# Performance work log

Measured on AMD Instinct MI355X. Metric: run time of the kernel, lower is better.

## Reference

```python
import jax, jax.numpy as jnp
import numpy as np

N, D, E, EDGE_DIM = 50000, 128, 800000, 3
NEG_SLOPE = 0.2
LN_EPS = 1e-5


def setup_inputs() -> dict:
    key = jax.random.key(0)
    ks = jax.random.split(key, 12)
    s = 1.0 / np.sqrt(D)
    return {
        "x": jax.random.normal(ks[0], (N, D), jnp.float32),
        "edge_index": jax.random.randint(ks[1], (2, E), 0, N, jnp.int32),
        "edge_attr": jax.random.normal(ks[2], (E, EDGE_DIM), jnp.float32),
        "W_l": jax.random.normal(ks[3], (D, D), jnp.float32) * s,
        "b_l": jnp.zeros((D,), jnp.float32),
        "W_r": jax.random.normal(ks[4], (D, D), jnp.float32) * s,
        "b_r": jnp.zeros((D,), jnp.float32),
        "W_e": jax.random.normal(ks[5], (EDGE_DIM, D), jnp.float32) * (1.0 / np.sqrt(EDGE_DIM)),
        "att": jax.random.normal(ks[6], (D,), jnp.float32) * s,
        "bias": jnp.zeros((D,), jnp.float32),
        "res_weight": jnp.array(0.1, jnp.float32),
        "ln_gamma": jnp.ones((D,), jnp.float32),
        "ln_beta": jnp.zeros((D,), jnp.float32),
    }


def reference(x, edge_index, edge_attr, W_l, b_l, W_r, b_r, W_e, att, bias,
              res_weight, ln_gamma, ln_beta):
    src, dst = edge_index[0], edge_index[1]
    # GATv2: lin_l on source, lin_r on target (heads=1, concat=False)
    x_l = x @ W_l + b_l            # [N, D]
    x_r = x @ W_r + b_r            # [N, D]
    e_emb = edge_attr @ W_e        # [E, D]
    # per-edge attention logits
    m = x_l[src] + x_r[dst] + e_emb                      # [E, D]
    m = jnp.where(m > 0, m, NEG_SLOPE * m)               # leaky_relu(0.2)
    alpha = m @ att                                       # [E]
    # segment softmax over destination nodes
    seg_max = jax.ops.segment_max(alpha, dst, num_segments=N)
    seg_max = jnp.where(jnp.isfinite(seg_max), seg_max, 0.0)
    ex = jnp.exp(alpha - seg_max[dst])
    seg_sum = jax.ops.segment_sum(ex, dst, num_segments=N)
    alpha = ex / (seg_sum[dst] + 1e-16)                   # [E]
    # weighted aggregation of transformed source features (dropout off / eval)
    msgs = x_l[src] * alpha[:, None]                      # [E, D]
    out = jax.ops.segment_sum(msgs, dst, num_segments=N) + bias  # [N, D]
    # residual + LayerNorm
    out = x + res_weight * out
    mu = jnp.mean(out, axis=-1, keepdims=True)
    var = jnp.mean(jnp.square(out - mu), axis=-1, keepdims=True)
    out = (out - mu) * jax.lax.rsqrt(var + LN_EPS)
    return out * ln_gamma + ln_beta
```

## Files before the change

### kernel.cpp

```cpp
#include <hip/hip_runtime.h>
#include <hip/hip_bf16.h>

#define N_NODES 50000
#define DIM 128
#define N_EDGES 800000
#define NEG_SLOPE 0.2f
#define LN_EPS 1e-5f
#define SCAN_BS 256
#define NB_SCAN ((N_NODES + SCAN_BS - 1) / SCAN_BS)
#define PADCAP (N_EDGES + 4 * N_NODES)


__global__ __launch_bounds__(256) void lin_kernel(
    const float* __restrict__ x,
    const float* __restrict__ Wl, const float* __restrict__ bl,
    const float* __restrict__ Wr, const float* __restrict__ br,
    __hip_bfloat16* __restrict__ xl_bf, float* __restrict__ xr)
{
    __shared__ float xs[8][DIM];
    const int node0 = blockIdx.x * 8;
    const int t = threadIdx.x;
    for (int i = t; i < 8 * DIM; i += 256) {
        int n = node0 + (i >> 7);
        xs[i >> 7][i & 127] = (n < N_NODES) ? x[(size_t)n * DIM + (i & 127)] : 0.f;
    }
    __syncthreads();
    const int d = t & 127;
    const bool is_l = (t < 128);
    const float* W = is_l ? Wl : Wr;
    const float* b = is_l ? bl : br;
    float acc[8];
#pragma unroll
    for (int i = 0; i < 8; i++) acc[i] = b[d];
#pragma unroll 4
    for (int k = 0; k < DIM; k++) {
        float w = W[k * DIM + d];
#pragma unroll
        for (int i = 0; i < 8; i++) acc[i] += xs[i][k] * w;
    }
#pragma unroll
    for (int i = 0; i < 8; i++) {
        int n = node0 + i;
        if (n < N_NODES) {
            if (is_l) xl_bf[(size_t)n * DIM + d] = __float2bfloat16(acc[i]);
            else      xr[(size_t)n * DIM + d] = acc[i];
        }
    }
}

__global__ __launch_bounds__(256) void hist_kernel(const int* __restrict__ dst_idx,
                                                   int* __restrict__ cnt) {
    int i = blockIdx.x * 256 + threadIdx.x;
    int e = i * 4;
    if (e + 4 <= N_EDGES) {
        const int4 d4 = *(const int4*)(dst_idx + e);
        atomicAdd(&cnt[d4.x], 1);
        atomicAdd(&cnt[d4.y], 1);
        atomicAdd(&cnt[d4.z], 1);
        atomicAdd(&cnt[d4.w], 1);
    } else {
        for (; e < N_EDGES; ++e) atomicAdd(&cnt[dst_idx[e]], 1);
    }
}

__global__ __launch_bounds__(SCAN_BS) void scan1_kernel(int* __restrict__ cnt,
                                                        int* __restrict__ partials) {
    __shared__ int sh[SCAN_BS];
    const int i = blockIdx.x * SCAN_BS + threadIdx.x;
    const int deg = (i < N_NODES) ? cnt[i] : 0;
    const int v = (deg + 3) & ~3;
    sh[threadIdx.x] = v;
    __syncthreads();
    for (int off = 1; off < SCAN_BS; off <<= 1) {
        int u = (threadIdx.x >= off) ? sh[threadIdx.x - off] : 0;
        __syncthreads();
        sh[threadIdx.x] += u;
        __syncthreads();
    }
    if (i < N_NODES) cnt[i] = sh[threadIdx.x] - v;
    if (threadIdx.x == SCAN_BS - 1) partials[blockIdx.x] = sh[threadIdx.x];
}

__global__ __launch_bounds__(SCAN_BS) void scan2_kernel(int* __restrict__ partials) {
    __shared__ int sh[SCAN_BS];
    const int t = threadIdx.x;
    const int v = (t < NB_SCAN) ? partials[t] : 0;
    sh[t] = v;
    __syncthreads();
    for (int off = 1; off < SCAN_BS; off <<= 1) {
        int u = (t >= off) ? sh[t - off] : 0;
        __syncthreads();
        sh[t] += u;
        __syncthreads();
    }
    if (t < NB_SCAN) partials[t] = sh[t] - v;
}

__global__ __launch_bounds__(SCAN_BS) void scan3_kernel(int* __restrict__ cnt,
                                                        const int* __restrict__ partials,
                                                        int* __restrict__ cursor) {
    const int i = blockIdx.x * SCAN_BS + threadIdx.x;
    if (i < N_NODES) {
        int rs = cnt[i] + partials[blockIdx.x];
        cnt[i] = rs;
        cursor[i] = rs;
    }
}

__global__ __launch_bounds__(256) void scatter_kernel(
    const int* __restrict__ src_idx, const int* __restrict__ dst_idx,
    const float* __restrict__ ea,
    int* __restrict__ cursor, float4* __restrict__ packed) {
    int e = blockIdx.x * 256 + threadIdx.x;
    if (e >= N_EDGES) return;
    int pos = atomicAdd(&cursor[dst_idx[e]], 1);
    float4 p;
    p.x = ea[(size_t)e * 3 + 0];
    p.y = ea[(size_t)e * 3 + 1];
    p.z = ea[(size_t)e * 3 + 2];
    p.w = __int_as_float(src_idx[e]);
    packed[pos] = p;
}

__global__ __launch_bounds__(256) void fused_node_kernel(
    const float* __restrict__ x, const __hip_bfloat16* __restrict__ xl_bf,
    const int* __restrict__ row_start, const int* __restrict__ cursor,
    const float4* __restrict__ packed,
    const float* __restrict__ We, const float* __restrict__ att,
    const float* __restrict__ bias, const float* __restrict__ rw_p,
    const float* __restrict__ gamma, const float* __restrict__ beta,
    float* __restrict__ out)
{
    const int v = blockIdx.x * 4 + (threadIdx.x >> 6);
    const int lane = threadIdx.x & 63;
    if (v >= N_NODES) return;
    const int begin = row_start[v];
    const int end   = cursor[v];
    const size_t nb = (size_t)v * DIM + 2 * lane;
    const int loff = 2 * lane;
    const float2 xrv = *(const float2*)&out[nb];
    const float2 at  = *(const float2*)&att[loff];
    const float2 we0 = *(const float2*)&We[0 * DIM + loff];
    const float2 we1 = *(const float2*)&We[1 * DIM + loff];
    const float2 we2 = *(const float2*)&We[2 * DIM + loff];

    float m = -3.4e38f, s = 0.f, a0 = 0.f, a1 = 0.f;
    int pos = begin;
    const int full_end = begin + ((end - begin) & ~3);

    float4 pk0, pk1, pk2, pk3;
    unsigned xu0, xu1, xu2, xu3;
    if (pos < full_end) {
        pk0 = packed[pos];     pk1 = packed[pos + 1];
        pk2 = packed[pos + 2]; pk3 = packed[pos + 3];
        xu0 = *(const unsigned*)&xl_bf[(size_t)__float_as_int(pk0.w) * DIM + loff];
        xu1 = *(const unsigned*)&xl_bf[(size_t)__float_as_int(pk1.w) * DIM + loff];
        xu2 = *(const unsigned*)&xl_bf[(size_t)__float_as_int(pk2.w) * DIM + loff];
        xu3 = *(const unsigned*)&xl_bf[(size_t)__float_as_int(pk3.w) * DIM + loff];
    }

    while (pos < full_end) {
        const int npos = pos + 4;
        const bool more = npos < full_end;
        float4 nk0, nk1, nk2, nk3;
        if (more) {
            nk0 = packed[npos];     nk1 = packed[npos + 1];
            nk2 = packed[npos + 2]; nk3 = packed[npos + 3];
        }
        const float xl00 = __uint_as_float(xu0 << 16), xl10 = __uint_as_float(xu0 & 0xffff0000u);
        const float xl01 = __uint_as_float(xu1 << 16), xl11 = __uint_as_float(xu1 & 0xffff0000u);
        const float xl02 = __uint_as_float(xu2 << 16), xl12 = __uint_as_float(xu2 & 0xffff0000u);
        const float xl03 = __uint_as_float(xu3 << 16), xl13 = __uint_as_float(xu3 & 0xffff0000u);

        float P0, P1, P2, P3;
        {
            float t0, t1;
            t0 = xl00 + xrv.x + pk0.x * we0.x + pk0.y * we1.x + pk0.z * we2.x;
            t1 = xl10 + xrv.y + pk0.x * we0.y + pk0.y * we1.y + pk0.z * we2.y;
            t0 = t0 > 0.f ? t0 : NEG_SLOPE * t0;  t1 = t1 > 0.f ? t1 : NEG_SLOPE * t1;
            P0 = t0 * at.x + t1 * at.y;
            t0 = xl01 + xrv.x + pk1.x * we0.x + pk1.y * we1.x + pk1.z * we2.x;
            t1 = xl11 + xrv.y + pk1.x * we0.y + pk1.y * we1.y + pk1.z * we2.y;
            t0 = t0 > 0.f ? t0 : NEG_SLOPE * t0;  t1 = t1 > 0.f ? t1 : NEG_SLOPE * t1;
            P1 = t0 * at.x + t1 * at.y;
            t0 = xl02 + xrv.x + pk2.x * we0.x + pk2.y * we1.x + pk2.z * we2.x;
            t1 = xl12 + xrv.y + pk2.x * we0.y + pk2.y * we1.y + pk2.z * we2.y;
            t0 = t0 > 0.f ? t0 : NEG_SLOPE * t0;  t1 = t1 > 0.f ? t1 : NEG_SLOPE * t1;
            P2 = t0 * at.x + t1 * at.y;
            t0 = xl03 + xrv.x + pk3.x * we0.x + pk3.y * we1.x + pk3.z * we2.x;
            t1 = xl13 + xrv.y + pk3.x * we0.y + pk3.y * we1.y + pk3.z * we2.y;
            t0 = t0 > 0.f ? t0 : NEG_SLOPE * t0;  t1 = t1 > 0.f ? t1 : NEG_SLOPE * t1;
            P3 = t0 * at.x + t1 * at.y;
        }
        unsigned nu0, nu1, nu2, nu3;
        if (more) {
            nu0 = *(const unsigned*)&xl_bf[(size_t)__float_as_int(nk0.w) * DIM + loff];
            nu1 = *(const unsigned*)&xl_bf[(size_t)__float_as_int(nk1.w) * DIM + loff];
            nu2 = *(const unsigned*)&xl_bf[(size_t)__float_as_int(nk2.w) * DIM + loff];
            nu3 = *(const unsigned*)&xl_bf[(size_t)__float_as_int(nk3.w) * DIM + loff];
        }
        const float tA0 = __shfl_xor(P0, 1, 64);
        const float tA1 = __shfl_xor(P1, 1, 64);
        const float tB0 = __shfl_xor(P2, 1, 64);
        const float tB1 = __shfl_xor(P3, 1, 64);
        const bool b0 = (lane & 1);
        float A = b0 ? (P1 + tA1) : (P0 + tA0);
        float B = b0 ? (P3 + tB1) : (P2 + tB0);
        const float tA = __shfl_xor(A, 2, 64);
        const float tB = __shfl_xor(B, 2, 64);
        float C = (lane & 2) ? (B + tB) : (A + tA);
        C += __shfl_xor(C, 4, 64);
        C += __shfl_xor(C, 8, 64);
        C += __shfl_xor(C, 16, 64);
        C += __shfl_xor(C, 32, 64);
        const int base = lane & ~3;
        const float p0 = __shfl(C, base + 0, 64);
        const float p1 = __shfl(C, base + 1, 64);
        const float p2 = __shfl(C, base + 2, 64);
        const float p3 = __shfl(C, base + 3, 64);

        const float pm = fmaxf(fmaxf(p0, p1), fmaxf(p2, p3));
        if (pm <= m + 8.f) {
            const float w0 = __expf(p0 - m), w1 = __expf(p1 - m);
            const float w2 = __expf(p2 - m), w3 = __expf(p3 - m);
            s  += (w0 + w1) + (w2 + w3);
            a0 += w0 * xl00 + w1 * xl01 + w2 * xl02 + w3 * xl03;
            a1 += w0 * xl10 + w1 * xl11 + w2 * xl12 + w3 * xl13;
        } else {
            const float mn = fmaxf(m, pm);
            const float f  = __expf(m - mn);
            const float w0 = __expf(p0 - mn), w1 = __expf(p1 - mn);
            const float w2 = __expf(p2 - mn), w3 = __expf(p3 - mn);
            s  = s  * f + (w0 + w1) + (w2 + w3);
            a0 = a0 * f + w0 * xl00 + w1 * xl01 + w2 * xl02 + w3 * xl03;
            a1 = a1 * f + w0 * xl10 + w1 * xl11 + w2 * xl12 + w3 * xl13;
            m = mn;
        }
        pk0 = nk0; pk1 = nk1; pk2 = nk2; pk3 = nk3;
        xu0 = nu0; xu1 = nu1; xu2 = nu2; xu3 = nu3;
        pos = npos;
    }

    for (; pos < end; ++pos) {
        const float4 pk = packed[pos];
        const int sn = __float_as_int(pk.w);
        const unsigned xu = *(const unsigned*)&xl_bf[(size_t)sn * DIM + loff];
        const float xl0 = __uint_as_float(xu << 16);
        const float xl1 = __uint_as_float(xu & 0xffff0000u);
        float t0 = xl0 + xrv.x + pk.x * we0.x + pk.y * we1.x + pk.z * we2.x;
        float t1 = xl1 + xrv.y + pk.x * we0.y + pk.y * we1.y + pk.z * we2.y;
        t0 = t0 > 0.f ? t0 : NEG_SLOPE * t0;
        t1 = t1 > 0.f ? t1 : NEG_SLOPE * t1;
        float p = t0 * at.x + t1 * at.y;
#pragma unroll
        for (int o = 32; o > 0; o >>= 1) p += __shfl_xor(p, o, 64);
        if (p <= m + 8.f) {
            const float w = __expf(p - m);
            s += w; a0 += w * xl0; a1 += w * xl1;
        } else {
            const float mn = fmaxf(m, p);
            const float f = __expf(m - mn);
            const float w = __expf(p - mn);
            s = s * f + w; a0 = a0 * f + w * xl0; a1 = a1 * f + w * xl1;
            m = mn;
        }
    }

    const float inv = 1.f / (s + 1e-16f);

    const float2 xv = *(const float2*)&x[nb];
    const float rw = rw_p[0];
    float v0 = xv.x + rw * (a0 * inv + bias[loff]);
    float v1 = xv.y + rw * (a1 * inv + bias[loff + 1]);
    float sum = v0 + v1;
#pragma unroll
    for (int o = 32; o > 0; o >>= 1) sum += __shfl_xor(sum, o, 64);
    const float mu = sum * (1.f / DIM);
    const float d0 = v0 - mu, d1 = v1 - mu;
    float q = d0 * d0 + d1 * d1;
#pragma unroll
    for (int o = 32; o > 0; o >>= 1) q += __shfl_xor(q, o, 64);
    const float rstd = rsqrtf(q * (1.f / DIM) + LN_EPS);
    float2 r;
    r.x = d0 * rstd * gamma[loff]     + beta[loff];
    r.y = d1 * rstd * gamma[loff + 1] + beta[loff + 1];
    *(float2*)&out[nb] = r;
}

extern "C" void kernel_launch(void* const* d_in, const int* in_sizes, int n_in,
                              void* d_out, int out_size, void* d_ws, size_t ws_size,
                              hipStream_t stream)
{
    const float* x    = (const float*)d_in[0];
    const int*   ei   = (const int*)d_in[1];
    const float* ea   = (const float*)d_in[2];
    const float* Wl   = (const float*)d_in[3];
    const float* bl   = (const float*)d_in[4];
    const float* Wr   = (const float*)d_in[5];
    const float* br   = (const float*)d_in[6];
    const float* We   = (const float*)d_in[7];
    const float* att  = (const float*)d_in[8];
    const float* bias = (const float*)d_in[9];
    const float* rw   = (const float*)d_in[10];
    const float* gmm  = (const float*)d_in[11];
    const float* bta  = (const float*)d_in[12];
    float* out = (float*)d_out;

    const int* src_idx = ei;
    const int* dst_idx = ei + N_EDGES;

    __hip_bfloat16* xl_bf = (__hip_bfloat16*)d_ws;
    float4* packed    = (float4*)(xl_bf + (size_t)N_NODES * DIM);
    int*   row_start  = (int*)(packed + PADCAP);
    int*   cursor     = row_start + N_NODES;
    int*   partials   = cursor + N_NODES;

    hipMemsetAsync(row_start, 0, (size_t)N_NODES * sizeof(int), stream);
    hist_kernel<<<(N_EDGES / 4 + 255) / 256, 256, 0, stream>>>(dst_idx, row_start);
    scan1_kernel<<<NB_SCAN, SCAN_BS, 0, stream>>>(row_start, partials);
    scan2_kernel<<<1, SCAN_BS, 0, stream>>>(partials);
    scan3_kernel<<<NB_SCAN, SCAN_BS, 0, stream>>>(row_start, partials, cursor);
    scatter_kernel<<<(N_EDGES + 255) / 256, 256, 0, stream>>>(src_idx, dst_idx, ea,
                                                              cursor, packed);
    lin_kernel<<<(N_NODES + 7) / 8, 256, 0, stream>>>(x, Wl, bl, Wr, br, xl_bf, out);
    fused_node_kernel<<<(N_NODES + 3) / 4, 256, 0, stream>>>(x, xl_bf, row_start, cursor,
                                                             packed,
                                                             We, att, bias, rw, gmm, bta, out);
}
```

Measured before the change: 366.2 us.

## Unroll edge loop to 8, merge scan kernels, enlarge lin_kernel node tile

The fused node kernel now handles edges in groups of 8 instead of 4. It issues all eight packed and bf16 gathers up front and drops the software-pipelined prefetch, and a 4-edge tail step runs before the scalar remainder. Row padding in the CSR scan moves from multiples of 4 to multiples of 8, and the packed capacity grows to match. scan2 and scan3 are merged so every block redoes the small partials scan, which removes one launch. lin_kernel computes 16 nodes per block with float2 shared reads to reuse each weight load more; the cost is more registers and less prefetch overlap in the gather loop.

```diff
diff --git a/kernel.cpp b/kernel.cpp
--- a/kernel.cpp
+++ b/kernel.cpp
@@ -8,7 +8,7 @@
 #define LN_EPS 1e-5f
 #define SCAN_BS 256
 #define NB_SCAN ((N_NODES + SCAN_BS - 1) / SCAN_BS)
-#define PADCAP (N_EDGES + 4 * N_NODES)
+#define PADCAP (N_EDGES + 7 * N_NODES)
 
 
 __global__ __launch_bounds__(256) void lin_kernel(
@@ -17,10 +17,10 @@
     const float* __restrict__ Wr, const float* __restrict__ br,
     __hip_bfloat16* __restrict__ xl_bf, float* __restrict__ xr)
 {
-    __shared__ float xs[8][DIM];
-    const int node0 = blockIdx.x * 8;
+    __shared__ float xs[16][DIM];
+    const int node0 = blockIdx.x * 16;
     const int t = threadIdx.x;
-    for (int i = t; i < 8 * DIM; i += 256) {
+    for (int i = t; i < 16 * DIM; i += 256) {
         int n = node0 + (i >> 7);
         xs[i >> 7][i & 127] = (n < N_NODES) ? x[(size_t)n * DIM + (i & 127)] : 0.f;
     }
@@ -29,17 +29,22 @@
     const bool is_l = (t < 128);
     const float* W = is_l ? Wl : Wr;
     const float* b = is_l ? bl : br;
-    float acc[8];
-#pragma unroll
-    for (int i = 0; i < 8; i++) acc[i] = b[d];
-#pragma unroll 4
-    for (int k = 0; k < DIM; k++) {
-        float w = W[k * DIM + d];
-#pragma unroll
-        for (int i = 0; i < 8; i++) acc[i] += xs[i][k] * w;
-    }
-#pragma unroll
-    for (int i = 0; i < 8; i++) {
+    float acc[16];
+#pragma unroll
+    for (int i = 0; i < 16; i++) acc[i] = b[d];
+#pragma unroll 2
+    for (int k = 0; k < DIM; k += 2) {
+        const float w0 = W[k * DIM + d];
+        const float w1 = W[(k + 1) * DIM + d];
+#pragma unroll
+        for (int i = 0; i < 16; i++) {
+            const float2 xv = *(const float2*)&xs[i][k];
+            acc[i] += xv.x * w0;
+            acc[i] += xv.y * w1;
+        }
+    }
+#pragma unroll
+    for (int i = 0; i < 16; i++) {
         int n = node0 + i;
         if (n < N_NODES) {
             if (is_l) xl_bf[(size_t)n * DIM + d] = __float2bfloat16(acc[i]);
@@ -68,7 +73,7 @@
     __shared__ int sh[SCAN_BS];
     const int i = blockIdx.x * SCAN_BS + threadIdx.x;
     const int deg = (i < N_NODES) ? cnt[i] : 0;
-    const int v = (deg + 3) & ~3;
+    const int v = (deg + 7) & ~7;
     sh[threadIdx.x] = v;
     __syncthreads();
     for (int off = 1; off < SCAN_BS; off <<= 1) {
@@ -81,11 +86,12 @@
     if (threadIdx.x == SCAN_BS - 1) partials[blockIdx.x] = sh[threadIdx.x];
 }
 
-__global__ __launch_bounds__(SCAN_BS) void scan2_kernel(int* __restrict__ partials) {
+__global__ __launch_bounds__(SCAN_BS) void scan23_kernel(int* __restrict__ cnt,
+                                                         const int* __restrict__ partials,
+                                                         int* __restrict__ cursor) {
     __shared__ int sh[SCAN_BS];
     const int t = threadIdx.x;
-    const int v = (t < NB_SCAN) ? partials[t] : 0;
-    sh[t] = v;
+    sh[t] = (t < NB_SCAN) ? partials[t] : 0;
     __syncthreads();
     for (int off = 1; off < SCAN_BS; off <<= 1) {
         int u = (t >= off) ? sh[t - off] : 0;
@@ -93,15 +99,10 @@
         sh[t] += u;
         __syncthreads();
     }
-    if (t < NB_SCAN) partials[t] = sh[t] - v;
-}
-
-__global__ __launch_bounds__(SCAN_BS) void scan3_kernel(int* __restrict__ cnt,
-                                                        const int* __restrict__ partials,
-                                                        int* __restrict__ cursor) {
-    const int i = blockIdx.x * SCAN_BS + threadIdx.x;
+    const int boff = (blockIdx.x == 0) ? 0 : sh[blockIdx.x - 1];
+    const int i = blockIdx.x * SCAN_BS + t;
     if (i < N_NODES) {
-        int rs = cnt[i] + partials[blockIdx.x];
+        const int rs = cnt[i] + boff;
         cnt[i] = rs;
         cursor[i] = rs;
     }
@@ -121,6 +122,15 @@
     p.w = __int_as_float(src_idx[e]);
     packed[pos] = p;
 }
+
+#define LOGIT(PX, K, XL0, XL1)                                               \
+    {                                                                        \
+        float t0 = (XL0) + xrv.x + (K).x * we0.x + (K).y * we1.x + (K).z * we2.x; \
+        float t1 = (XL1) + xrv.y + (K).x * we0.y + (K).y * we1.y + (K).z * we2.y; \
+        t0 = t0 > 0.f ? t0 : NEG_SLOPE * t0;                                 \
+        t1 = t1 > 0.f ? t1 : NEG_SLOPE * t1;                                 \
+        PX = t0 * at.x + t1 * at.y;                                          \
+    }
 
 __global__ __launch_bounds__(256) void fused_node_kernel(
     const float* __restrict__ x, const __hip_bfloat16* __restrict__ xl_bf,
@@ -146,79 +156,122 @@
 
     float m = -3.4e38f, s = 0.f, a0 = 0.f, a1 = 0.f;
     int pos = begin;
-    const int full_end = begin + ((end - begin) & ~3);
-
-    float4 pk0, pk1, pk2, pk3;
-    unsigned xu0, xu1, xu2, xu3;
-    if (pos < full_end) {
-        pk0 = packed[pos];     pk1 = packed[pos + 1];
-        pk2 = packed[pos + 2]; pk3 = packed[pos + 3];
-        xu0 = *(const unsigned*)&xl_bf[(size_t)__float_as_int(pk0.w) * DIM + loff];
-        xu1 = *(const unsigned*)&xl_bf[(size_t)__float_as_int(pk1.w) * DIM + loff];
-        xu2 = *(const unsigned*)&xl_bf[(size_t)__float_as_int(pk2.w) * DIM + loff];
-        xu3 = *(const unsigned*)&xl_bf[(size_t)__float_as_int(pk3.w) * DIM + loff];
-    }
-
-    while (pos < full_end) {
-        const int npos = pos + 4;
-        const bool more = npos < full_end;
-        float4 nk0, nk1, nk2, nk3;
-        if (more) {
-            nk0 = packed[npos];     nk1 = packed[npos + 1];
-            nk2 = packed[npos + 2]; nk3 = packed[npos + 3];
-        }
+    const int deg = end - begin;
+    const int full8 = begin + (deg & ~7);
+
+    for (; pos < full8; pos += 8) {
+        const float4 k0 = packed[pos + 0], k1 = packed[pos + 1];
+        const float4 k2 = packed[pos + 2], k3 = packed[pos + 3];
+        const float4 k4 = packed[pos + 4], k5 = packed[pos + 5];
+        const float4 k6 = packed[pos + 6], k7 = packed[pos + 7];
+        const unsigned xu0 = *(const unsigned*)&xl_bf[(size_t)__float_as_int(k0.w) * DIM + loff];
+        const unsigned xu1 = *(const unsigned*)&xl_bf[(size_t)__float_as_int(k1.w) * DIM + loff];
+        const unsigned xu2 = *(const unsigned*)&xl_bf[(size_t)__float_as_int(k2.w) * DIM + loff];
+        const unsigned xu3 = *(const unsigned*)&xl_bf[(size_t)__float_as_int(k3.w) * DIM + loff];
+        const unsigned xu4 = *(const unsigned*)&xl_bf[(size_t)__float_as_int(k4.w) * DIM + loff];
+        const unsigned xu5 = *(const unsigned*)&xl_bf[(size_t)__float_as_int(k5.w) * DIM + loff];
+        const unsigned xu6 = *(const unsigned*)&xl_bf[(size_t)__float_as_int(k6.w) * DIM + loff];
+        const unsigned xu7 = *(const unsigned*)&xl_bf[(size_t)__float_as_int(k7.w) * DIM + loff];
         const float xl00 = __uint_as_float(xu0 << 16), xl10 = __uint_as_float(xu0 & 0xffff0000u);
         const float xl01 = __uint_as_float(xu1 << 16), xl11 = __uint_as_float(xu1 & 0xffff0000u);
         const float xl02 = __uint_as_float(xu2 << 16), xl12 = __uint_as_float(xu2 & 0xffff0000u);
         const float xl03 = __uint_as_float(xu3 << 16), xl13 = __uint_as_float(xu3 & 0xffff0000u);
-
+        const float xl04 = __uint_as_float(xu4 << 16), xl14 = __uint_as_float(xu4 & 0xffff0000u);
+        const float xl05 = __uint_as_float(xu5 << 16), xl15 = __uint_as_float(xu5 & 0xffff0000u);
+        const float xl06 = __uint_as_float(xu6 << 16), xl16 = __uint_as_float(xu6 & 0xffff0000u);
+        const float xl07 = __uint_as_float(xu7 << 16), xl17 = __uint_as_float(xu7 & 0xffff0000u);
+
+        float P0, P1, P2, P3, P4, P5, P6, P7;
+        LOGIT(P0, k0, xl00, xl10)  LOGIT(P1, k1, xl01, xl11)
+        LOGIT(P2, k2, xl02, xl12)  LOGIT(P3, k3, xl03, xl13)
+        LOGIT(P4, k4, xl04, xl14)  LOGIT(P5, k5, xl05, xl15)
+        LOGIT(P6, k6, xl06, xl16)  LOGIT(P7, k7, xl07, xl17)
+
+        const bool b1 = (lane & 1), b2 = (lane & 2), b4 = (lane & 4);
+        float A0, A1, A2, A3, B0, B1, G;
+        {
+            const float q0 = __shfl_xor(P0, 1, 64), q1 = __shfl_xor(P1, 1, 64);
+            const float q2 = __shfl_xor(P2, 1, 64), q3 = __shfl_xor(P3, 1, 64);
+            const float q4 = __shfl_xor(P4, 1, 64), q5 = __shfl_xor(P5, 1, 64);
+            const float q6 = __shfl_xor(P6, 1, 64), q7 = __shfl_xor(P7, 1, 64);
+            A0 = b1 ? (P1 + q1) : (P0 + q0);
+            A1 = b1 ? (P3 + q3) : (P2 + q2);
+            A2 = b1 ? (P5 + q5) : (P4 + q4);
+            A3 = b1 ? (P7 + q7) : (P6 + q6);
+        }
+        {
+            const float q0 = __shfl_xor(A0, 2, 64), q1 = __shfl_xor(A1, 2, 64);
+            const float q2 = __shfl_xor(A2, 2, 64), q3 = __shfl_xor(A3, 2, 64);
+            B0 = b2 ? (A1 + q1) : (A0 + q0);
+            B1 = b2 ? (A3 + q3) : (A2 + q2);
+        }
+        {
+            const float q0 = __shfl_xor(B0, 4, 64), q1 = __shfl_xor(B1, 4, 64);
+            G = b4 ? (B1 + q1) : (B0 + q0);
+        }
+        G += __shfl_xor(G, 8, 64);
+        G += __shfl_xor(G, 16, 64);
+        G += __shfl_xor(G, 32, 64);
+        const float p0 = __shfl(G, 0, 64), p1 = __shfl(G, 1, 64);
+        const float p2 = __shfl(G, 2, 64), p3 = __shfl(G, 3, 64);
+        const float p4 = __shfl(G, 4, 64), p5 = __shfl(G, 5, 64);
+        const float p6 = __shfl(G, 6, 64), p7 = __shfl(G, 7, 64);
+
+        const float pm = fmaxf(fmaxf(fmaxf(p0, p1), fmaxf(p2, p3)),
+                               fmaxf(fmaxf(p4, p5), fmaxf(p6, p7)));
+        if (pm <= m + 8.f) {
+            const float w0 = __expf(p0 - m), w1 = __expf(p1 - m);
+            const float w2 = __expf(p2 - m), w3 = __expf(p3 - m);
+            const float w4 = __expf(p4 - m), w5 = __expf(p5 - m);
+            const float w6 = __expf(p6 - m), w7 = __expf(p7 - m);
+            s  += ((w0 + w1) + (w2 + w3)) + ((w4 + w5) + (w6 + w7));
+            a0 += (w0 * xl00 + w1 * xl01 + w2 * xl02 + w3 * xl03)
+                + (w4 * xl04 + w5 * xl05 + w6 * xl06 + w7 * xl07);
+            a1 += (w0 * xl10 + w1 * xl11 + w2 * xl12 + w3 * xl13)
+                + (w4 * xl14 + w5 * xl15 + w6 * xl16 + w7 * xl17);
+        } else {
+            const float mn = fmaxf(m, pm);
+            const float f  = __expf(m - mn);
+            const float w0 = __expf(p0 - mn), w1 = __expf(p1 - mn);
+            const float w2 = __expf(p2 - mn), w3 = __expf(p3 - mn);
+            const float w4 = __expf(p4 - mn), w5 = __expf(p5 - mn);
+            const float w6 = __expf(p6 - mn), w7 = __expf(p7 - mn);
+            s  = s  * f + ((w0 + w1) + (w2 + w3)) + ((w4 + w5) + (w6 + w7));
+            a0 = a0 * f + (w0 * xl00 + w1 * xl01 + w2 * xl02 + w3 * xl03)
+                        + (w4 * xl04 + w5 * xl05 + w6 * xl06 + w7 * xl07);
+            a1 = a1 * f + (w0 * xl10 + w1 * xl11 + w2 * xl12 + w3 * xl13)
+                        + (w4 * xl14 + w5 * xl15 + w6 * xl16 + w7 * xl17);
+            m = mn;
+        }
+    }
+
+    if (end - pos >= 4) {
+        const float4 k0 = packed[pos + 0], k1 = packed[pos + 1];
+        const float4 k2 = packed[pos + 2], k3 = packed[pos + 3];
+        const unsigned xu0 = *(const unsigned*)&xl_bf[(size_t)__float_as_int(k0.w) * DIM + loff];
+        const unsigned xu1 = *(const unsigned*)&xl_bf[(size_t)__float_as_int(k1.w) * DIM + loff];
+        const unsigned xu2 = *(const unsigned*)&xl_bf[(size_t)__float_as_int(k2.w) * DIM + loff];
+        const unsigned xu3 = *(const unsigned*)&xl_bf[(size_t)__float_as_int(k3.w) * DIM + loff];
+        const float xl00 = __uint_as_float(xu0 << 16), xl10 = __uint_as_float(xu0 & 0xffff0000u);
+        const float xl01 = __uint_as_float(xu1 << 16), xl11 = __uint_as_float(xu1 & 0xffff0000u);
+        const float xl02 = __uint_as_float(xu2 << 16), xl12 = __uint_as_float(xu2 & 0xffff0000u);
+        const float xl03 = __uint_as_float(xu3 << 16), xl13 = __uint_as_float(xu3 & 0xffff0000u);
         float P0, P1, P2, P3;
-        {
-            float t0, t1;
-            t0 = xl00 + xrv.x + pk0.x * we0.x + pk0.y * we1.x + pk0.z * we2.x;
-            t1 = xl10 + xrv.y + pk0.x * we0.y + pk0.y * we1.y + pk0.z * we2.y;
-            t0 = t0 > 0.f ? t0 : NEG_SLOPE * t0;  t1 = t1 > 0.f ? t1 : NEG_SLOPE * t1;
-            P0 = t0 * at.x + t1 * at.y;
-            t0 = xl01 + xrv.x + pk1.x * we0.x + pk1.y * we1.x + pk1.z * we2.x;
-            t1 = xl11 + xrv.y + pk1.x * we0.y + pk1.y * we1.y + pk1.z * we2.y;
-            t0 = t0 > 0.f ? t0 : NEG_SLOPE * t0;  t1 = t1 > 0.f ? t1 : NEG_SLOPE * t1;
-            P1 = t0 * at.x + t1 * at.y;
-            t0 = xl02 + xrv.x + pk2.x * we0.x + pk2.y * we1.x + pk2.z * we2.x;
-            t1 = xl12 + xrv.y + pk2.x * we0.y + pk2.y * we1.y + pk2.z * we2.y;
-            t0 = t0 > 0.f ? t0 : NEG_SLOPE * t0;  t1 = t1 > 0.f ? t1 : NEG_SLOPE * t1;
-            P2 = t0 * at.x + t1 * at.y;
-            t0 = xl03 + xrv.x + pk3.x * we0.x + pk3.y * we1.x + pk3.z * we2.x;
-            t1 = xl13 + xrv.y + pk3.x * we0.y + pk3.y * we1.y + pk3.z * we2.y;
-            t0 = t0 > 0.f ? t0 : NEG_SLOPE * t0;  t1 = t1 > 0.f ? t1 : NEG_SLOPE * t1;
-            P3 = t0 * at.x + t1 * at.y;
-        }
-        unsigned nu0, nu1, nu2, nu3;
-        if (more) {
-            nu0 = *(const unsigned*)&xl_bf[(size_t)__float_as_int(nk0.w) * DIM + loff];
-            nu1 = *(const unsigned*)&xl_bf[(size_t)__float_as_int(nk1.w) * DIM + loff];
-            nu2 = *(const unsigned*)&xl_bf[(size_t)__float_as_int(nk2.w) * DIM + loff];
-            nu3 = *(const unsigned*)&xl_bf[(size_t)__float_as_int(nk3.w) * DIM + loff];
-        }
-        const float tA0 = __shfl_xor(P0, 1, 64);
-        const float tA1 = __shfl_xor(P1, 1, 64);
-        const float tB0 = __shfl_xor(P2, 1, 64);
-        const float tB1 = __shfl_xor(P3, 1, 64);
+        LOGIT(P0, k0, xl00, xl10)  LOGIT(P1, k1, xl01, xl11)
+        LOGIT(P2, k2, xl02, xl12)  LOGIT(P3, k3, xl03, xl13)
+        const float tA0 = __shfl_xor(P0, 1, 64), tA1 = __shfl_xor(P1, 1, 64);
+        const float tB0 = __shfl_xor(P2, 1, 64), tB1 = __shfl_xor(P3, 1, 64);
         const bool b0 = (lane & 1);
         float A = b0 ? (P1 + tA1) : (P0 + tA0);
         float B = b0 ? (P3 + tB1) : (P2 + tB0);
-        const float tA = __shfl_xor(A, 2, 64);
-        const float tB = __shfl_xor(B, 2, 64);
+        const float tA = __shfl_xor(A, 2, 64), tB = __shfl_xor(B, 2, 64);
         float C = (lane & 2) ? (B + tB) : (A + tA);
         C += __shfl_xor(C, 4, 64);
         C += __shfl_xor(C, 8, 64);
         C += __shfl_xor(C, 16, 64);
         C += __shfl_xor(C, 32, 64);
-        const int base = lane & ~3;
-        const float p0 = __shfl(C, base + 0, 64);
-        const float p1 = __shfl(C, base + 1, 64);
-        const float p2 = __shfl(C, base + 2, 64);
-        const float p3 = __shfl(C, base + 3, 64);
-
+        const float p0 = __shfl(C, 0, 64), p1 = __shfl(C, 1, 64);
+        const float p2 = __shfl(C, 2, 64), p3 = __shfl(C, 3, 64);
         const float pm = fmaxf(fmaxf(p0, p1), fmaxf(p2, p3));
         if (pm <= m + 8.f) {
             const float w0 = __expf(p0 - m), w1 = __expf(p1 - m);
@@ -236,22 +289,16 @@
             a1 = a1 * f + w0 * xl10 + w1 * xl11 + w2 * xl12 + w3 * xl13;
             m = mn;
         }
-        pk0 = nk0; pk1 = nk1; pk2 = nk2; pk3 = nk3;
-        xu0 = nu0; xu1 = nu1; xu2 = nu2; xu3 = nu3;
-        pos = npos;
+        pos += 4;
     }
 
     for (; pos < end; ++pos) {
         const float4 pk = packed[pos];
-        const int sn = __float_as_int(pk.w);
-        const unsigned xu = *(const unsigned*)&xl_bf[(size_t)sn * DIM + loff];
+        const unsigned xu = *(const unsigned*)&xl_bf[(size_t)__float_as_int(pk.w) * DIM + loff];
         const float xl0 = __uint_as_float(xu << 16);
         const float xl1 = __uint_as_float(xu & 0xffff0000u);
-        float t0 = xl0 + xrv.x + pk.x * we0.x + pk.y * we1.x + pk.z * we2.x;
-        float t1 = xl1 + xrv.y + pk.x * we0.y + pk.y * we1.y + pk.z * we2.y;
-        t0 = t0 > 0.f ? t0 : NEG_SLOPE * t0;
-        t1 = t1 > 0.f ? t1 : NEG_SLOPE * t1;
-        float p = t0 * at.x + t1 * at.y;
+        float p;
+        LOGIT(p, pk, xl0, xl1)
 #pragma unroll
         for (int o = 32; o > 0; o >>= 1) p += __shfl_xor(p, o, 64);
         if (p <= m + 8.f) {
@@ -318,11 +365,10 @@
     hipMemsetAsync(row_start, 0, (size_t)N_NODES * sizeof(int), stream);
     hist_kernel<<<(N_EDGES / 4 + 255) / 256, 256, 0, stream>>>(dst_idx, row_start);
     scan1_kernel<<<NB_SCAN, SCAN_BS, 0, stream>>>(row_start, partials);
-    scan2_kernel<<<1, SCAN_BS, 0, stream>>>(partials);
-    scan3_kernel<<<NB_SCAN, SCAN_BS, 0, stream>>>(row_start, partials, cursor);
+    scan23_kernel<<<NB_SCAN, SCAN_BS, 0, stream>>>(row_start, partials, cursor);
     scatter_kernel<<<(N_EDGES + 255) / 256, 256, 0, stream>>>(src_idx, dst_idx, ea,
                                                               cursor, packed);
-    lin_kernel<<<(N_NODES + 7) / 8, 256, 0, stream>>>(x, Wl, bl, Wr, br, xl_bf, out);
+    lin_kernel<<<(N_NODES + 15) / 16, 256, 0, stream>>>(x, Wl, bl, Wr, br, xl_bf, out);
     fused_node_kernel<<<(N_NODES + 3) / 4, 256, 0, stream>>>(x, xl_bf, row_start, cursor,
                                                              packed,
                                                              We, att, bias, rw, gmm, bta, out);
```

Measured after the change: 349.6 us. 1.05x faster.
